# Kernel tuning notes

Hardware: AMD Instinct MI355X
Metric: run time of the kernel (lower is better)

Reference implementation:

```python
import jax, jax.numpy as jnp
import numpy as np

EPS = 1e-3        # Memory.eps distance threshold
MOMENTUM = 0.999  # Memory.momentum
N, F, M = 500000, 256, 1024


def setup_inputs() -> dict:
    key = jax.random.key(0)
    k1, k2, k3, k4, k5 = jax.random.split(key, 5)
    return {
        "points": jax.random.normal(k1, (M, 3), dtype=jnp.float32),
        "descriptors": jax.random.normal(k2, (M, F), dtype=jnp.float32),
        # learned/stateful memory bank (params/buffers of the module)
        "mem_points": jax.random.normal(k3, (N, 3), dtype=jnp.float32),
        "mem_descriptors": jax.random.normal(k4, (N, F), dtype=jnp.float32),
        "usage": jax.random.randint(k5, (N,), 0, 1000, dtype=jnp.int32),
    }


def _moving(x, m):
    # faithful to Memory.moving: x*m + (1-m)*x  (== x, kept as written)
    return x * m + (1.0 - m) * x


def reference(points, descriptors, mem_points, mem_descriptors, usage):
    # ---- point_address: cdist (p=2) + argmin nearest neighbor ----
    # squared-distance expansion; [M, N] matrix
    d2 = (jnp.sum(points * points, axis=-1)[:, None]
          + jnp.sum(mem_points * mem_points, axis=-1)[None, :]
          - 2.0 * points @ mem_points.T)
    dist = jnp.sqrt(jnp.maximum(d2, 1e-12))
    dmin = jnp.min(dist, axis=-1)
    idx = jnp.argmin(dist, axis=-1)            # [M]
    mask = dmin > EPS                          # queries with no near match

    # ---- topk eviction: lowest-usage slots, assigned in query order ----
    # torch: idx[mask] = usage.topk(k=mask.sum(), largest=False).indices
    # static-shape equivalent: take top-M least-used, select first cumsum(mask)
    _, evict = jax.lax.top_k(-usage, points.shape[0])  # [M] least-used slots
    rank = jnp.cumsum(mask.astype(jnp.int32)) - 1      # position among masked
    idx = jnp.where(mask, evict[rank], idx)

    momentum = jnp.where(mask, 0.0, MOMENTUM)[:, None]  # [M, 1]

    # ---- write: usage bump + momentum scatter-update ----
    usage_new = usage.at[idx].add(1)
    pts_new = mem_points.at[idx].set(_moving(mem_points[idx], momentum))
    desc_new = mem_descriptors.at[idx].set(_moving(mem_descriptors[idx], momentum))

    out = jnp.concatenate([pts_new, desc_new], axis=1)  # [N, 3+F]
    return out, usage_new, idx
```

## Files before the change

kernel.cpp:

```cpp
#include <hip/hip_runtime.h>

#define N_TOT   500000
#define M_Q     1024
#define QB      16
#define NSPLIT  16
#define CAND_MAX 8192

#define ARGMIN_BLKS 1024
#define HIST_BLKS   32
#define USAGE_BLKS  64
#define CROWS       16
#define COPY_BLKS   (N_TOT / CROWS)
#define MEGA_BLKS   (ARGMIN_BLKS + HIST_BLKS + USAGE_BLKS + COPY_BLKS)
#define HIST_CHUNK  (N_TOT / HIST_BLKS)

static const unsigned OUT_ROWS  = 259u * (unsigned)N_TOT;
static const unsigned OUT_USAGE = OUT_ROWS;
static const unsigned OUT_IDX   = OUT_ROWS + (unsigned)N_TOT;

#define WS_PARTKEY 0
#define WS_PARTIDX 65536
#define WS_HISTP   131072
#define WS_V       262144
#define WS_CNT     262148
#define WS_KEYS    262152

__global__ __launch_bounds__(256) void k_mega(
    const float* __restrict__ pts,  const float* __restrict__ mpts,
    const float* __restrict__ mdesc, const int* __restrict__ usage,
    float* __restrict__ out,
    float* __restrict__ partKey, int* __restrict__ partIdx,
    int* __restrict__ histPart)
{
    __shared__ float smem[CROWS * 259];
    const int b   = blockIdx.x;
    const int tid = threadIdx.x;

    if (b < ARGMIN_BLKS) {
        const int qb = b & 63;
        const int ns = b >> 6;
        const int qbase = qb * QB;
        const int chunk = N_TOT / NSPLIT;
        const int n0 = ns * chunk;
        const int n1 = n0 + chunk;

        float* qs = smem;
        float* wk = smem + 64;
        int*   wi = (int*)(smem + 192);
        if (tid < QB * 3) qs[tid] = pts[qbase * 3 + tid];
        __syncthreads();

        float qx[QB], qy[QB], qz[QB];
#pragma unroll
        for (int i = 0; i < QB; i++) { qx[i] = qs[3*i]; qy[i] = qs[3*i+1]; qz[i] = qs[3*i+2]; }

        float bk[QB]; int bi[QB];
#pragma unroll
        for (int i = 0; i < QB; i++) { bk[i] = INFINITY; bi[i] = 0x7fffffff; }

        for (int n = n0 + tid; n < n1; n += 256) {
            float x = mpts[3*n+0], y = mpts[3*n+1], z = mpts[3*n+2];
            float h = 0.5f * (x*x + y*y + z*z);
#pragma unroll
            for (int i = 0; i < QB; i++) {
                float key = h - x*qx[i] - y*qy[i] - z*qz[i];
                bool lt = key < bk[i];
                bk[i] = lt ? key : bk[i];
                bi[i] = lt ? n   : bi[i];
            }
        }

        const int lane = tid & 63;
        const int wv   = tid >> 6;
#pragma unroll
        for (int off = 32; off > 0; off >>= 1) {
#pragma unroll
            for (int i = 0; i < QB; i++) {
                float ok = __shfl_down(bk[i], off, 64);
                int   oi = __shfl_down(bi[i], off, 64);
                if (ok < bk[i] || (ok == bk[i] && oi < bi[i])) { bk[i] = ok; bi[i] = oi; }
            }
        }
        if (lane == 0) {
#pragma unroll
            for (int i = 0; i < QB; i++) { wk[wv*QB + i] = bk[i]; wi[wv*QB + i] = bi[i]; }
        }
        __syncthreads();
        if (tid < QB) {
            float k = wk[tid]; int ix = wi[tid];
#pragma unroll
            for (int w = 1; w < 4; w++) {
                float ok = wk[w*QB + tid]; int oi = wi[w*QB + tid];
                if (ok < k || (ok == k && oi < ix)) { k = ok; ix = oi; }
            }
            partKey[(qbase + tid) * NSPLIT + ns] = k;
            partIdx[(qbase + tid) * NSPLIT + ns] = ix;
        }
    } else if (b < ARGMIN_BLKS + HIST_BLKS) {
        const int hb = b - ARGMIN_BLKS;
        const int r0 = hb * HIST_CHUNK;
        const int r1 = r0 + HIST_CHUNK;
        int* lh = (int*)smem;
#pragma unroll
        for (int i = 0; i < 4; i++) lh[tid + i * 256] = 0;
        __syncthreads();
        for (int n = r0 + tid; n < r1; n += 256) {
            unsigned v = (unsigned)usage[n];
            if (v > 1023u) v = 1023u;
            atomicAdd(&lh[v], 1);
        }
        __syncthreads();
#pragma unroll
        for (int i = 0; i < 4; i++) {
            int bin = tid + i * 256;
            histPart[hb * 1024 + bin] = lh[bin];
        }
    } else if (b < ARGMIN_BLKS + HIST_BLKS + USAGE_BLKS) {
        const int ub = b - ARGMIN_BLKS - HIST_BLKS;
        const int4* u4 = (const int4*)usage;
        float4* o4 = (float4*)(out + OUT_USAGE);
        const int TOT4 = N_TOT / 4;
        for (int g = ub * 256 + tid; g < TOT4; g += USAGE_BLKS * 256) {
            int4 u = u4[g];
            o4[g] = make_float4((float)u.x, (float)u.y, (float)u.z, (float)u.w);
        }
    } else {
        const int cb = b - (ARGMIN_BLKS + HIST_BLKS + USAGE_BLKS);
        const int n0 = cb * CROWS;
        const float4* src = (const float4*)(mdesc + (size_t)n0 * 256);
#pragma unroll
        for (int it = 0; it < 4; it++) {
            int g = tid + it * 256;
            float4 v = src[g];
            int e = g * 4;
            int r = e >> 8;
            int c = e & 255;
            float* d = smem + r * 259 + 3 + c;
            d[0] = v.x; d[1] = v.y; d[2] = v.z; d[3] = v.w;
        }
        if (tid < CROWS * 3) {
            int r = tid / 3, c = tid - r * 3;
            smem[r * 259 + c] = mpts[(size_t)n0 * 3 + tid];
        }
        __syncthreads();
        float4* dst4 = (float4*)(out + (size_t)cb * (CROWS * 259));
        const float4* s4 = (const float4*)smem;
#pragma unroll
        for (int it = 0; it < 5; it++) {
            int g = tid + it * 256;
            if (g < CROWS * 259 / 4) dst4[g] = s4[g];
        }
    }
}

__global__ __launch_bounds__(1024) void k_scanV(
    const int* __restrict__ histPart, int* __restrict__ Vout, int* __restrict__ cnt)
{
    __shared__ int scan[1024];
    const int t = threadIdx.x;
    int h = 0;
#pragma unroll
    for (int b = 0; b < HIST_BLKS; b++) h += histPart[b * 1024 + t];
    scan[t] = h; __syncthreads();
    for (int off = 1; off < 1024; off <<= 1) {
        int add = (t >= off) ? scan[t - off] : 0;
        __syncthreads();
        scan[t] += add;
        __syncthreads();
    }
    int cum  = scan[t] - h;
    int cumN = scan[t];
    if (cum < M_Q && cumN >= M_Q) { *Vout = t; *cnt = 0; }
}

__global__ __launch_bounds__(256) void k_collect(
    const int* __restrict__ usage, const int* __restrict__ Vp,
    int* __restrict__ cnt, unsigned* __restrict__ keys)
{
    const int V = *Vp;
    const int stride = gridDim.x * 256;
    for (int n = blockIdx.x * 256 + threadIdx.x; n < N_TOT; n += stride) {
        int u = usage[n];
        if (u <= V) {
            int p = atomicAdd(cnt, 1);
            if (p < CAND_MAX) keys[p] = ((unsigned)u << 19) | (unsigned)n;
        }
    }
}

__global__ __launch_bounds__(1024) void k_final(
    const float* __restrict__ pts,
    const float* __restrict__ partKey, const int* __restrict__ partIdx,
    const int* __restrict__ cntP, const unsigned* __restrict__ keysG,
    float* __restrict__ out)
{
    __shared__ unsigned keys[CAND_MAX];
    __shared__ int      mscan[1024];
    const int t = threadIdx.x;

    float bk = INFINITY; int bi = 0x7fffffff;
#pragma unroll
    for (int s = 0; s < NSPLIT; s++) {
        float k = partKey[t * NSPLIT + s];
        int   i = partIdx[t * NSPLIT + s];
        if (k < bk) { bk = k; bi = i; }
    }
    float px = pts[3*t], py = pts[3*t+1], pz = pts[3*t+2];
    float d2 = px*px + py*py + pz*pz + 2.0f * bk;
    const bool mask = d2 > 1e-6f;

    int C = *cntP; if (C > CAND_MAX) C = CAND_MAX;
    int P2 = 1; while (P2 < C) P2 <<= 1;
    for (int p = t; p < P2; p += 1024) keys[p] = (p < C) ? keysG[p] : 0xFFFFFFFFu;
    __syncthreads();

    for (int k = 2; k <= P2; k <<= 1) {
        for (int j = k >> 1; j > 0; j >>= 1) {
            for (int i = t; i < P2; i += 1024) {
                int ixj = i ^ j;
                if (ixj > i) {
                    unsigned a = keys[i], bb = keys[ixj];
                    bool up = ((i & k) == 0);
                    if ((a > bb) == up) { keys[i] = bb; keys[ixj] = a; }
                }
            }
            __syncthreads();
        }
    }

    mscan[t] = mask ? 1 : 0; __syncthreads();
    for (int off = 1; off < 1024; off <<= 1) {
        int add = (t >= off) ? mscan[t - off] : 0;
        __syncthreads();
        mscan[t] += add;
        __syncthreads();
    }
    int rank = mscan[t] - 1;
    int idx = mask ? (int)(keys[rank] & 0x7FFFFu) : bi;
    out[(size_t)OUT_IDX + (size_t)t] = (float)idx;
    atomicAdd(out + OUT_USAGE + idx, 1.0f);
}

extern "C" void kernel_launch(void* const* d_in, const int* in_sizes, int n_in,
                              void* d_out, int out_size, void* d_ws, size_t ws_size,
                              hipStream_t stream)
{
    (void)in_sizes; (void)n_in; (void)out_size; (void)ws_size;
    const float* pts   = (const float*)d_in[0];
    const float* mpts  = (const float*)d_in[2];
    const float* mdesc = (const float*)d_in[3];
    const int*   usage = (const int*)d_in[4];
    float* out = (float*)d_out;

    char* ws = (char*)d_ws;
    float*    partKey  = (float*)(ws + WS_PARTKEY);
    int*      partIdx  = (int*)(ws + WS_PARTIDX);
    int*      histPart = (int*)(ws + WS_HISTP);
    int*      Vp       = (int*)(ws + WS_V);
    int*      cnt      = (int*)(ws + WS_CNT);
    unsigned* keys     = (unsigned*)(ws + WS_KEYS);

    k_mega<<<MEGA_BLKS, 256, 0, stream>>>(pts, mpts, mdesc, usage, out,
                                          partKey, partIdx, histPart);
    k_scanV<<<1, 1024, 0, stream>>>(histPart, Vp, cnt);
    k_collect<<<64, 256, 0, stream>>>(usage, Vp, cnt, keys);
    k_final<<<1, 1024, 0, stream>>>(pts, partKey, partIdx, cnt, keys, out);
}
```

Baseline: 331.7 us.

## Make copy blocks persistent with double-buffered LDS tiles and nontemporal stores

Replaces 31250 one-tile copy blocks with 625 persistent blocks that each loop over 50 tiles. The blocks alternate between two LDS buffers so a tile's loads can overlap the previous tile's stores with only one barrier per tile. Output writes use nontemporal stores to reduce cache pollution. Copy blocks are moved to the front of the grid so the bandwidth-bound work starts first. The cost is fewer blocks for the copy and a dependence on the single-barrier double-buffer reuse being race-free.

```diff
diff --git a/kernel.cpp b/kernel.cpp
--- a/kernel.cpp
+++ b/kernel.cpp
@@ -6,13 +6,17 @@
 #define NSPLIT  16
 #define CAND_MAX 8192
 
+#define CROWS       16
+#define NTILES      (N_TOT / CROWS)
+#define COPY_BLKS   625
+#define TILES_PER_B (NTILES / COPY_BLKS)
 #define ARGMIN_BLKS 1024
 #define HIST_BLKS   32
 #define USAGE_BLKS  64
-#define CROWS       16
-#define COPY_BLKS   (N_TOT / CROWS)
-#define MEGA_BLKS   (ARGMIN_BLKS + HIST_BLKS + USAGE_BLKS + COPY_BLKS)
+#define MEGA_BLKS   (COPY_BLKS + ARGMIN_BLKS + HIST_BLKS + USAGE_BLKS)
 #define HIST_CHUNK  (N_TOT / HIST_BLKS)
+
+#define TILE_F      (CROWS * 259)
 
 static const unsigned OUT_ROWS  = 259u * (unsigned)N_TOT;
 static const unsigned OUT_USAGE = OUT_ROWS;
@@ -25,6 +29,8 @@
 #define WS_CNT     262148
 #define WS_KEYS    262152
 
+typedef float f4v __attribute__((ext_vector_type(4)));
+
 __global__ __launch_bounds__(256) void k_mega(
     const float* __restrict__ pts,  const float* __restrict__ mpts,
     const float* __restrict__ mdesc, const int* __restrict__ usage,
@@ -32,13 +38,48 @@
     float* __restrict__ partKey, int* __restrict__ partIdx,
     int* __restrict__ histPart)
 {
-    __shared__ float smem[CROWS * 259];
+    __shared__ float smem[2 * TILE_F];
     const int b   = blockIdx.x;
     const int tid = threadIdx.x;
 
-    if (b < ARGMIN_BLKS) {
-        const int qb = b & 63;
-        const int ns = b >> 6;
+    if (b < COPY_BLKS) {
+        for (int t = 0; t < TILES_PER_B; ++t) {
+            const int tile = b * TILES_PER_B + t;
+            const int n0   = tile * CROWS;
+            float* L = smem + (t & 1) * TILE_F;
+
+            const float4* src = (const float4*)(mdesc + (size_t)n0 * 256);
+            float4 v[4];
+#pragma unroll
+            for (int it = 0; it < 4; it++) v[it] = src[tid + it * 256];
+            float pv = (tid < CROWS * 3) ? mpts[(size_t)n0 * 3 + tid] : 0.0f;
+
+#pragma unroll
+            for (int it = 0; it < 4; it++) {
+                int g = tid + it * 256;
+                int r = g >> 6;
+                int c = (g & 63) << 2;
+                float* d = L + r * 259 + 3 + c;
+                d[0] = v[it].x; d[1] = v[it].y; d[2] = v[it].z; d[3] = v[it].w;
+            }
+            if (tid < CROWS * 3) {
+                int r = tid / 3, c = tid - r * 3;
+                L[r * 259 + c] = pv;
+            }
+            __syncthreads();
+
+            f4v* dst4 = (f4v*)(out + (size_t)tile * TILE_F);
+            const f4v* s4 = (const f4v*)L;
+#pragma unroll
+            for (int it = 0; it < 5; it++) {
+                int g = tid + it * 256;
+                if (g < TILE_F / 4) __builtin_nontemporal_store(s4[g], dst4 + g);
+            }
+        }
+    } else if (b < COPY_BLKS + ARGMIN_BLKS) {
+        const int rb = b - COPY_BLKS;
+        const int qb = rb & 63;
+        const int ns = rb >> 6;
         const int qbase = qb * QB;
         const int chunk = N_TOT / NSPLIT;
         const int n0 = ns * chunk;
@@ -96,8 +137,8 @@
             partKey[(qbase + tid) * NSPLIT + ns] = k;
             partIdx[(qbase + tid) * NSPLIT + ns] = ix;
         }
-    } else if (b < ARGMIN_BLKS + HIST_BLKS) {
-        const int hb = b - ARGMIN_BLKS;
+    } else if (b < COPY_BLKS + ARGMIN_BLKS + HIST_BLKS) {
+        const int hb = b - COPY_BLKS - ARGMIN_BLKS;
         const int r0 = hb * HIST_CHUNK;
         const int r1 = r0 + HIST_CHUNK;
         int* lh = (int*)smem;
@@ -115,40 +156,14 @@
             int bin = tid + i * 256;
             histPart[hb * 1024 + bin] = lh[bin];
         }
-    } else if (b < ARGMIN_BLKS + HIST_BLKS + USAGE_BLKS) {
-        const int ub = b - ARGMIN_BLKS - HIST_BLKS;
+    } else {
+        const int ub = b - COPY_BLKS - ARGMIN_BLKS - HIST_BLKS;
         const int4* u4 = (const int4*)usage;
         float4* o4 = (float4*)(out + OUT_USAGE);
         const int TOT4 = N_TOT / 4;
         for (int g = ub * 256 + tid; g < TOT4; g += USAGE_BLKS * 256) {
             int4 u = u4[g];
             o4[g] = make_float4((float)u.x, (float)u.y, (float)u.z, (float)u.w);
-        }
-    } else {
-        const int cb = b - (ARGMIN_BLKS + HIST_BLKS + USAGE_BLKS);
-        const int n0 = cb * CROWS;
-        const float4* src = (const float4*)(mdesc + (size_t)n0 * 256);
-#pragma unroll
-        for (int it = 0; it < 4; it++) {
-            int g = tid + it * 256;
-            float4 v = src[g];
-            int e = g * 4;
-            int r = e >> 8;
-            int c = e & 255;
-            float* d = smem + r * 259 + 3 + c;
-            d[0] = v.x; d[1] = v.y; d[2] = v.z; d[3] = v.w;
-        }
-        if (tid < CROWS * 3) {
-            int r = tid / 3, c = tid - r * 3;
-            smem[r * 259 + c] = mpts[(size_t)n0 * 3 + tid];
-        }
-        __syncthreads();
-        float4* dst4 = (float4*)(out + (size_t)cb * (CROWS * 259));
-        const float4* s4 = (const float4*)smem;
-#pragma unroll
-        for (int it = 0; it < 5; it++) {
-            int g = tid + it * 256;
-            if (g < CROWS * 259 / 4) dst4[g] = s4[g];
         }
     }
 }
```

Result: slower. 347.7 us (+4.8%).
